# Kernel tuning notes

Hardware: AMD Instinct MI355X
Metric: run time of the kernel (lower is better)

The kernel has to match this reference:

```python
import jax, jax.numpy as jnp
import numpy as np

NODE_F = 8      # node_features
HID = 128       # hidden_dim
HEADS = 8       # nn.MultiheadAttention num_heads
OUT = 256       # output_dim
MAX_ATOMS = 4096  # max_pocket_atoms
NEIGHBOR_RADIUS = 3.0   # _compute_surface_scores neighbor_radius


def setup_inputs() -> dict:
    key = jax.random.key(0)
    ks = jax.random.split(key, 16)
    N, M = 16384, 32
    x = jax.random.normal(ks[0], (N, NODE_F), dtype=jnp.float32)
    pos = jax.random.normal(ks[1], (N, 3), dtype=jnp.float32) * 10.0
    ligand_pos = jax.random.normal(ks[2], (M, 3), dtype=jnp.float32) * 3.0

    def lin(k, fan_in, fan_out):
        return jax.random.normal(k, (fan_in, fan_out), dtype=jnp.float32) / np.sqrt(fan_in)

    return {
        'x': x, 'pos': pos, 'ligand_pos': ligand_pos,
        'W_node': lin(ks[3], NODE_F, HID), 'b_node': jnp.zeros((HID,), jnp.float32),
        'Wq': lin(ks[4], HID, HID), 'bq': jnp.zeros((HID,), jnp.float32),
        'Wk': lin(ks[5], HID, HID), 'bk': jnp.zeros((HID,), jnp.float32),
        'Wv': lin(ks[6], HID, HID), 'bv': jnp.zeros((HID,), jnp.float32),
        'Wo': lin(ks[7], HID, HID), 'bo': jnp.zeros((HID,), jnp.float32),
        'W1': lin(ks[8], HID, OUT), 'b1': jnp.zeros((OUT,), jnp.float32),
        'W2': lin(ks[9], OUT, OUT), 'b2': jnp.zeros((OUT,), jnp.float32),
    }


def _select_binding_site(pos, ligand_pos, k):
    # select_by_binding_site_proximity: distance-to-ligand-center + surface scores, topk
    lig_center = jnp.mean(ligand_pos, axis=0)                       # [3]
    d_lig = jnp.linalg.norm(pos - lig_center, axis=1)               # [N]
    # _compute_surface_scores: cdist(pos,pos) < 3.0, count neighbors (minus self)
    sq = jnp.sum(pos * pos, axis=1)                                 # [N]
    d2 = sq[:, None] + sq[None, :] - 2.0 * (pos @ pos.T)            # [N,N] squared distances
    neighbor_counts = jnp.sum(d2 < NEIGHBOR_RADIUS ** 2, axis=1) - 1
    surface = 1.0 / (neighbor_counts.astype(jnp.float32) + 1.0)
    scores = 1.0 / (1.0 + d_lig / 5.0) + 0.5 * surface
    _, idx = jax.lax.top_k(scores, k)                               # largest=True
    return idx


def reference(x, pos, ligand_pos, W_node, b_node, Wq, bq, Wk, bk, Wv, bv, Wo, bo, W1, b1, W2, b2):
    # N > max_pocket_atoms -> smart selection (adaptive with ligand_pos => binding_site)
    idx = _select_binding_site(pos, ligand_pos, MAX_ATOMS)
    xs = x[idx]                                                     # [K, NODE_F]

    # node embedding (E3 net call fails in the original -> h = node_embedding(x))
    h = xs @ W_node + b_node                                        # [K, HID]

    # MultiheadAttention over the single (batch=None) sequence, eval mode (no dropout)
    K = MAX_ATOMS
    dh = HID // HEADS
    q = (h @ Wq + bq).reshape(K, HEADS, dh).transpose(1, 0, 2)      # [H,K,dh]
    k_ = (h @ Wk + bk).reshape(K, HEADS, dh).transpose(1, 0, 2)
    v = (h @ Wv + bv).reshape(K, HEADS, dh).transpose(1, 0, 2)
    attn = jax.nn.softmax(jnp.einsum('hqd,hkd->hqk', q, k_) / np.sqrt(dh), axis=-1)
    av = jnp.einsum('hqk,hkd->hqd', attn, v).transpose(1, 0, 2).reshape(K, HID)
    h_att = av @ Wo + bo                                            # [K, HID]

    # global mean pool + output projection (Linear-ReLU-Linear)
    pooled = jnp.mean(h_att, axis=0)                                # [HID]
    out = jax.nn.relu(pooled @ W1 + b1) @ W2 + b2                   # [OUT]
    return out
```

## Files before the change

kernel.cpp:

```cpp
#include <hip/hip_runtime.h>
#include <cstdint>
#include <cstddef>

#define NPTS 16384
#define KSEL 4096
#define HIDDEN 128
#define NHEADS 8
#define DHEAD 16
#define OUTD 256
#define NSLICE 4
#define FCAP 262144
#define LCAP 2048
#define TAU 0.15f

typedef __attribute__((ext_vector_type(8))) short bf16x8;
typedef __attribute__((ext_vector_type(4))) float f32x4;
typedef __attribute__((ext_vector_type(16))) float f32x16;

#if defined(__has_builtin)
#if __has_builtin(__builtin_amdgcn_exp2f)
#define E2(x) __builtin_amdgcn_exp2f(x)
#endif
#endif
#ifndef E2
#define E2(x) exp2f(x)
#endif

constexpr size_t OFF_PA    = 1024;
constexpr size_t OFF_PB    = OFF_PA  + (size_t)NPTS*32;
constexpr size_t OFF_SQ    = OFF_PB  + (size_t)NPTS*32;
constexpr size_t OFF_DL    = OFF_SQ  + (size_t)NPTS*4;
constexpr size_t OFF_CNT   = OFF_DL  + (size_t)NPTS*4;
constexpr size_t OFF_NFLAG = OFF_CNT + (size_t)NPTS*4;
constexpr size_t OFF_FLG   = OFF_NFLAG + 1024;
constexpr size_t OFF_SEL   = OFF_FLG + (size_t)FCAP*4;
constexpr size_t SZ_PK     = (size_t)NHEADS*KSEL*32*2;
constexpr size_t OFF_QPK   = OFF_SEL + (size_t)KSEL*4;
constexpr size_t OFF_KPK   = OFF_QPK + SZ_PK;
constexpr size_t OFF_V     = OFF_KPK + SZ_PK;
constexpr size_t OFF_LP    = OFF_V  + (size_t)KSEL*HIDDEN*4;
constexpr size_t OFF_WP    = OFF_LP + (size_t)NHEADS*KSEL*NSLICE*4;
constexpr size_t OFF_PAV   = OFF_WP + (size_t)NHEADS*KSEL*NSLICE*4;

__device__ __forceinline__ unsigned short f2bf(float f) {
    union { float f; unsigned u; } v; v.f = f;
    unsigned r = v.u + 0x7fffu + ((v.u >> 16) & 1u);
    return (unsigned short)(r >> 16);
}
__device__ __forceinline__ float bf2f(unsigned short h) {
    union { unsigned u; float f; } v; v.u = ((unsigned)h) << 16;
    return v.f;
}

__global__ void __launch_bounds__(256) k_prep(const float* __restrict__ pos, const float* __restrict__ lig, int M,
                       unsigned short* __restrict__ pa, unsigned short* __restrict__ pb,
                       float* __restrict__ sq, float* __restrict__ dl,
                       int* __restrict__ cnt, unsigned int* __restrict__ nflag, float* __restrict__ pav) {
    __shared__ float ls[128];
    __shared__ float ctr[3];
    int tid = threadIdx.x;
    int i = blockIdx.x * 256 + tid;
    cnt[i] = 0;
    if (i == 0) *nflag = 0;
    if (blockIdx.x == 0 && tid < HIDDEN) pav[tid] = 0.f;
    for (int k = tid; k < 3 * M; k += 256) ls[k] = lig[k];
    __syncthreads();
    if (tid < 3) {
        float s = 0.f;
        for (int k = 0; k < M; k++) s += ls[k * 3 + tid];
        ctr[tid] = s / (float)M;
    }
    __syncthreads();
    float x = pos[i*3+0], y = pos[i*3+1], z = pos[i*3+2];
    float s = (x*x + y*y) + z*z;
    sq[i] = s;
    float dx = x - ctr[0], dy = y - ctr[1], dz = z - ctr[2];
    dl[i] = sqrtf((dx*dx + dy*dy) + dz*dz);
    unsigned short xh = f2bf(x); float xr = bf2f(xh); float xl = x - xr;
    unsigned short yh = f2bf(y); float yr = bf2f(yh); float yl = y - yr;
    unsigned short zh = f2bf(z); float zr = bf2f(zh); float zl = z - zr;
    unsigned short xlb = f2bf(xl), ylb = f2bf(yl), zlb = f2bf(zl);
    unsigned short xhA = f2bf(-2.f*xr), xlA = f2bf(-2.f*xl);
    unsigned short yhA = f2bf(-2.f*yr), ylA = f2bf(-2.f*yl);
    unsigned short zhA = f2bf(-2.f*zr), zlA = f2bf(-2.f*zl);
    unsigned short sih = f2bf(s);
    unsigned short sil = f2bf(s - bf2f(sih));
    unsigned short one = f2bf(1.0f);
    union { unsigned short s[16]; float4 f[2]; } A, B;
    A.s[0]=xhA; A.s[1]=xhA; A.s[2]=xlA;
    A.s[3]=yhA; A.s[4]=yhA; A.s[5]=ylA;
    A.s[6]=zhA; A.s[7]=zhA; A.s[8]=zlA;
    A.s[9]=xlA; A.s[10]=ylA; A.s[11]=zlA;
    A.s[12]=sih; A.s[13]=sil; A.s[14]=one; A.s[15]=one;
    B.s[0]=xh;  B.s[1]=xlb;  B.s[2]=xh;
    B.s[3]=yh;  B.s[4]=ylb;  B.s[5]=yh;
    B.s[6]=zh;  B.s[7]=zlb;  B.s[8]=zh;
    B.s[9]=xlb; B.s[10]=ylb; B.s[11]=zlb;
    B.s[12]=one; B.s[13]=one; B.s[14]=sih; B.s[15]=sil;
    float4* pad = (float4*)(pa + (size_t)i * 16);
    pad[0] = A.f[0]; pad[1] = A.f[1];
    float4* pbd = (float4*)(pb + (size_t)i * 16);
    pbd[0] = B.f[0]; pbd[1] = B.f[1];
}

__global__ void __launch_bounds__(256) k_neighbor(
        const unsigned short* __restrict__ pa, const unsigned short* __restrict__ pb,
        int* __restrict__ cnt, unsigned int* __restrict__ flg, unsigned int* __restrict__ nflag) {
    __shared__ unsigned short js[256 * 24];
    __shared__ unsigned int fbuf[LCAP];
    __shared__ unsigned int fcnt, fbase;
    int tid = threadIdx.x;
    if (tid == 0) fcnt = 0;
    int lane = tid & 63, w = tid >> 6;
    int half = lane >> 5, il = lane & 31;
    int i = blockIdx.x * 128 + w * 32 + il;
    bf16x8 bfrag = *(const bf16x8*)(pb + (size_t)i * 16 + half * 8);
    int jb0 = blockIdx.y * 1024;
    int acc = 0;
    for (int chv = 0; chv < 4; chv++) {
        int jb = jb0 + chv * 256;
        __syncthreads();
        {
            const float4* src = (const float4*)(pa + (size_t)(jb + tid) * 16);
            float4 v0 = src[0], v1 = src[1];
            float4* dst = (float4*)&js[tid * 24];
            dst[0] = v0; dst[1] = v1;
        }
        __syncthreads();
        #pragma unroll 2
        for (int t = 0; t < 8; t++) {
            bf16x8 afrag = *(const bf16x8*)&js[(t * 32 + il) * 24 + half * 8];
            f32x16 c = {0.f,0.f,0.f,0.f,0.f,0.f,0.f,0.f,0.f,0.f,0.f,0.f,0.f,0.f,0.f,0.f};
            c = __builtin_amdgcn_mfma_f32_32x32x16_bf16(afrag, bfrag, c, 0, 0, 0);
            int cs = 0, cl = 0;
            #pragma unroll
            for (int r = 0; r < 16; r++) {
                cs += (c[r] < 9.0f - TAU);
                cl += (c[r] < 9.0f + TAU);
            }
            if (cl == cs) {
                acc += cs;
            } else {
                unsigned jt9 = (unsigned)((jb >> 5) + t);
                unsigned xx = atomicAdd(&fcnt, 1u);
                if (xx < LCAP) fbuf[xx] = ((unsigned)i << 10) | (jt9 << 1) | (unsigned)half;
            }
        }
    }
    acc += __shfl_xor(acc, 32);
    if (half == 0) atomicAdd(&cnt[i], acc);
    __syncthreads();
    if (tid == 0) {
        unsigned cf = fcnt; if (cf > LCAP) cf = LCAP;
        fcnt = cf;
        fbase = atomicAdd(nflag, cf);
    }
    __syncthreads();
    unsigned cf = fcnt, fb = fbase;
    for (unsigned xx = tid; xx < cf; xx += 256) {
        unsigned di = fb + xx;
        if (di < FCAP) flg[di] = fbuf[xx];
    }
}

__global__ void __launch_bounds__(256) k_fixup(const float* __restrict__ pos, const float* __restrict__ sq,
        const unsigned int* __restrict__ flg, const unsigned int* __restrict__ nflag,
        int* __restrict__ cnt) {
    int nf = (int)*nflag; if (nf > FCAP) nf = FCAP;
    for (int idx = blockIdx.x * 256 + threadIdx.x; idx < nf; idx += gridDim.x * 256) {
        unsigned pr = flg[idx];
        int i = (int)(pr >> 10);
        int jt = (int)((pr >> 1) & 511u) << 5;
        int half = (int)(pr & 1u);
        float xi = pos[i*3+0], yi = pos[i*3+1], zi = pos[i*3+2];
        float si = sq[i];
        int add = 0;
        #pragma unroll
        for (int r = 0; r < 16; r++) {
            int j = jt + (r & 3) + 8 * (r >> 2) + 4 * half;
            float xj = pos[j*3+0], yj = pos[j*3+1], zj = pos[j*3+2];
            float dot = fmaf(xi, xj, fmaf(yi, yj, zi * zj));
            float d2 = (si + sq[j]) - 2.0f * dot;
            add += (d2 < 9.0f);
        }
        atomicAdd(&cnt[i], add);
    }
}

__global__ void __launch_bounds__(1024) k_select(const float* __restrict__ dl, const int* __restrict__ cnt,
                                                 int* __restrict__ sel) {
    __shared__ unsigned int sk[NPTS];
    __shared__ int hist[256];
    __shared__ int scan2[256];
    __shared__ unsigned int s_prefix;
    __shared__ int s_rem, s_eqtot, s_nout, s_digit, s_cgt;
    int tid = threadIdx.x;
    for (int i = tid; i < NPTS; i += 1024) {
        float score = 1.0f / (1.0f + dl[i] / 5.0f) + 0.5f * (1.0f / (float)cnt[i]);
        unsigned int u = __float_as_uint(score);
        sk[i] = u ^ ((u & 0x80000000u) ? 0xFFFFFFFFu : 0x80000000u);
    }
    if (tid == 0) { s_prefix = 0; s_rem = KSEL; s_nout = 0; s_eqtot = 0; }
    __syncthreads();
    for (int p = 0; p < 4; p++) {
        int sh = 24 - 8 * p;
        if (tid < 256) hist[tid] = 0;
        __syncthreads();
        unsigned int pref = s_prefix;
        int shp = (p == 0) ? 0 : (32 - 8 * p);
        for (int i = tid; i < NPTS; i += 1024) {
            unsigned int key = sk[i];
            bool m = (p == 0) || ((key >> shp) == pref);
            if (m) atomicAdd(&hist[(key >> sh) & 255], 1);
        }
        __syncthreads();
        if (tid < 256) scan2[tid] = hist[tid];
        __syncthreads();
        for (int off = 1; off < 256; off <<= 1) {
            int v = 0;
            if (tid < 256) { v = scan2[tid]; if (tid + off < 256) v += scan2[tid + off]; }
            __syncthreads();
            if (tid < 256) scan2[tid] = v;
            __syncthreads();
        }
        int rem = s_rem;
        if (tid < 256) {
            int hi = scan2[tid];
            int lo = hi - hist[tid];
            if (hi >= rem && lo < rem) { s_digit = tid; s_cgt = lo; }
        }
        __syncthreads();
        if (tid == 0) {
            s_prefix = (s_prefix << 8) | (unsigned int)s_digit;
            s_rem = rem - s_cgt;
            if (p == 3) s_eqtot = hist[s_digit];
        }
        __syncthreads();
    }
    unsigned int T = s_prefix;
    int need_eq = s_rem;
    for (int i = tid; i < NPTS; i += 1024)
        if (sk[i] > T) sel[atomicAdd(&s_nout, 1)] = i;
    __syncthreads();
    if (s_eqtot == need_eq) {
        for (int i = tid; i < NPTS; i += 1024)
            if (sk[i] == T) sel[atomicAdd(&s_nout, 1)] = i;
    } else {
        for (int i = tid; i < NPTS; i += 1024) {
            if (sk[i] == T) {
                int rank = 0;
                for (int j = 0; j < i; j++) rank += (sk[j] == T);
                if (rank < need_eq) sel[atomicAdd(&s_nout, 1)] = i;
            }
        }
    }
}

__global__ void __launch_bounds__(256) k_qkv(const float* __restrict__ x, const int* __restrict__ sel,
        const float* __restrict__ Wn, const float* __restrict__ bn,
        const float* __restrict__ Wq, const float* __restrict__ bq,
        const float* __restrict__ Wk, const float* __restrict__ bk,
        const float* __restrict__ Wv, const float* __restrict__ bv,
        unsigned short* __restrict__ qpk, unsigned short* __restrict__ kpk,
        float* __restrict__ vg) {
    __shared__ float xs[32][8];
    __shared__ __align__(16) float hs[32][HIDDEN];
    int tid = threadIdx.x;
    int r0 = blockIdx.x * 32;
    { int rr = tid >> 3, cc = tid & 7; xs[rr][cc] = x[(size_t)sel[r0 + rr] * 8 + cc]; }
    __syncthreads();
    int d = tid & 127, hr = tid >> 7;
    {
        float wn[8];
        #pragma unroll
        for (int c = 0; c < 8; c++) wn[c] = Wn[c * HIDDEN + d];
        float b = bn[d];
        #pragma unroll
        for (int r = 0; r < 16; r++) {
            int row = hr * 16 + r;
            float a = b;
            #pragma unroll
            for (int c = 0; c < 8; c++) a = fmaf(xs[row][c], wn[c], a);
            hs[row][d] = a;
        }
    }
    __syncthreads();
    int hh = d >> 4, dd = d & 15;
    float acc[16];
    {
        float b = bq[d];
        #pragma unroll
        for (int r = 0; r < 16; r++) acc[r] = b;
        for (int c = 0; c < HIDDEN; c += 4) {
            float w0 = Wq[(c+0)*HIDDEN+d], w1 = Wq[(c+1)*HIDDEN+d], w2 = Wq[(c+2)*HIDDEN+d], w3 = Wq[(c+3)*HIDDEN+d];
            #pragma unroll
            for (int r = 0; r < 16; r++) {
                float4 h4 = *(const float4*)&hs[hr*16+r][c];
                float a = acc[r];
                a = fmaf(h4.x, w0, a); a = fmaf(h4.y, w1, a); a = fmaf(h4.z, w2, a); a = fmaf(h4.w, w3, a);
                acc[r] = a;
            }
        }
        #pragma unroll
        for (int r = 0; r < 16; r++) {
            float val = acc[r] * 0.36067376022224085f;
            unsigned short hi = f2bf(val);
            unsigned short lo = f2bf(val - bf2f(hi));
            size_t idx = ((size_t)(hh * KSEL) + r0 + hr*16 + r) * 32 + dd;
            qpk[idx] = hi; qpk[idx + 16] = lo;
        }
    }
    {
        float b = bk[d];
        #pragma unroll
        for (int r = 0; r < 16; r++) acc[r] = b;
        for (int c = 0; c < HIDDEN; c += 4) {
            float w0 = Wk[(c+0)*HIDDEN+d], w1 = Wk[(c+1)*HIDDEN+d], w2 = Wk[(c+2)*HIDDEN+d], w3 = Wk[(c+3)*HIDDEN+d];
            #pragma unroll
            for (int r = 0; r < 16; r++) {
                float4 h4 = *(const float4*)&hs[hr*16+r][c];
                float a = acc[r];
                a = fmaf(h4.x, w0, a); a = fmaf(h4.y, w1, a); a = fmaf(h4.z, w2, a); a = fmaf(h4.w, w3, a);
                acc[r] = a;
            }
        }
        #pragma unroll
        for (int r = 0; r < 16; r++) {
            float val = acc[r];
            unsigned short hi = f2bf(val);
            unsigned short lo = f2bf(val - bf2f(hi));
            size_t idx = ((size_t)(hh * KSEL) + r0 + hr*16 + r) * 32 + dd;
            kpk[idx] = hi; kpk[idx + 16] = lo;
        }
    }
    {
        float b = bv[d];
        #pragma unroll
        for (int r = 0; r < 16; r++) acc[r] = b;
        for (int c = 0; c < HIDDEN; c += 4) {
            float w0 = Wv[(c+0)*HIDDEN+d], w1 = Wv[(c+1)*HIDDEN+d], w2 = Wv[(c+2)*HIDDEN+d], w3 = Wv[(c+3)*HIDDEN+d];
            #pragma unroll
            for (int r = 0; r < 16; r++) {
                float4 h4 = *(const float4*)&hs[hr*16+r][c];
                float a = acc[r];
                a = fmaf(h4.x, w0, a); a = fmaf(h4.y, w1, a); a = fmaf(h4.z, w2, a); a = fmaf(h4.w, w3, a);
                acc[r] = a;
            }
        }
        #pragma unroll
        for (int r = 0; r < 16; r++) vg[(size_t)(r0 + hr*16 + r) * HIDDEN + d] = acc[r];
    }
}

__global__ void __launch_bounds__(256) k_attn_l(
        const unsigned short* __restrict__ qpk, const unsigned short* __restrict__ kpk,
        float* __restrict__ lp) {
    __shared__ unsigned short smem[256 * 40];
    int tid = threadIdx.x;
    int ks = blockIdx.x, yg = blockIdx.y, h = blockIdx.z;
    size_t hb = (size_t)h * KSEL;
    int lane = tid & 63, w = tid >> 6;
    int n = lane & 15, g = lane >> 4;
    int q0w = yg * 64 + w * 16;
    bf16x8 afrag = *(const bf16x8*)(qpk + (hb + q0w + n) * 32 + g * 8);
    float l0 = 0.f, l1 = 0.f, l2 = 0.f, l3 = 0.f;
    int b1off = (g & 1) * 8;
    int b2off = 16 + g * 8;
    for (int kc = 0; kc < 4; kc++) {
        __syncthreads();
        {
            int krow = ks * 1024 + kc * 256 + tid;
            const float4* src = (const float4*)(kpk + (hb + krow) * 32);
            float4 a0 = src[0], a1 = src[1], a2 = src[2], a3 = src[3];
            float4* dst = (float4*)&smem[tid * 40];
            dst[0] = a0; dst[1] = a1; dst[2] = a2; dst[3] = a3;
        }
        __syncthreads();
        #pragma unroll 4
        for (int t = 0; t < 16; t++) {
            const unsigned short* rowp = &smem[(t * 16 + n) * 40];
            bf16x8 b1 = *(const bf16x8*)(rowp + b1off);
            bf16x8 b2 = {0,0,0,0,0,0,0,0};
            if (g < 2) b2 = *(const bf16x8*)(rowp + b2off);
            f32x4 c = {0.f, 0.f, 0.f, 0.f};
            c = __builtin_amdgcn_mfma_f32_16x16x32_bf16(afrag, b1, c, 0, 0, 0);
            c = __builtin_amdgcn_mfma_f32_16x16x32_bf16(afrag, b2, c, 0, 0, 0);
            l0 += E2(c[0]); l1 += E2(c[1]); l2 += E2(c[2]); l3 += E2(c[3]);
        }
    }
    #pragma unroll
    for (int m = 1; m < 16; m <<= 1) {
        l0 += __shfl_xor(l0, m); l1 += __shfl_xor(l1, m);
        l2 += __shfl_xor(l2, m); l3 += __shfl_xor(l3, m);
    }
    if (n == 0) {
        size_t base = (hb + q0w + g * 4) * NSLICE + ks;
        lp[base]            = l0; lp[base + NSLICE]     = l1;
        lp[base + 2*NSLICE] = l2; lp[base + 3*NSLICE]   = l3;
    }
}

__global__ void __launch_bounds__(256) k_attn_w(
        const unsigned short* __restrict__ qpk, const unsigned short* __restrict__ kpk,
        const float* __restrict__ lp, float* __restrict__ wp) {
    __shared__ unsigned short smem[256 * 40];
    __shared__ float rls[256];
    int tid = threadIdx.x;
    int qs = blockIdx.x, yg = blockIdx.y, h = blockIdx.z;
    size_t hb = (size_t)h * KSEL;
    int lane = tid & 63, w = tid >> 6;
    int n = lane & 15, g = lane >> 4;
    int j0w = yg * 64 + w * 16;
    bf16x8 afrag = *(const bf16x8*)(kpk + (hb + j0w + n) * 32 + g * 8);
    float w0 = 0.f, w1 = 0.f, w2 = 0.f, w3 = 0.f;
    int b1off = (g & 1) * 8;
    int b2off = 16 + g * 8;
    for (int qc = 0; qc < 4; qc++) {
        __syncthreads();
        {
            int qrow = qs * 1024 + qc * 256 + tid;
            const float4* src = (const float4*)(qpk + (hb + qrow) * 32);
            float4 a0 = src[0], a1 = src[1], a2 = src[2], a3 = src[3];
            float4* dst = (float4*)&smem[tid * 40];
            dst[0] = a0; dst[1] = a1; dst[2] = a2; dst[3] = a3;
            float4 p = ((const float4*)lp)[hb + qrow];
            rls[tid] = 1.0f / ((p.x + p.y) + (p.z + p.w));
        }
        __syncthreads();
        #pragma unroll 4
        for (int t = 0; t < 16; t++) {
            const unsigned short* rowp = &smem[(t * 16 + n) * 40];
            bf16x8 b1 = *(const bf16x8*)(rowp + b1off);
            bf16x8 b2 = {0,0,0,0,0,0,0,0};
            if (g < 2) b2 = *(const bf16x8*)(rowp + b2off);
            f32x4 c = {0.f, 0.f, 0.f, 0.f};
            c = __builtin_amdgcn_mfma_f32_16x16x32_bf16(afrag, b1, c, 0, 0, 0);
            c = __builtin_amdgcn_mfma_f32_16x16x32_bf16(afrag, b2, c, 0, 0, 0);
            float rv = rls[t * 16 + n];
            w0 = fmaf(E2(c[0]), rv, w0); w1 = fmaf(E2(c[1]), rv, w1);
            w2 = fmaf(E2(c[2]), rv, w2); w3 = fmaf(E2(c[3]), rv, w3);
        }
    }
    #pragma unroll
    for (int m = 1; m < 16; m <<= 1) {
        w0 += __shfl_xor(w0, m); w1 += __shfl_xor(w1, m);
        w2 += __shfl_xor(w2, m); w3 += __shfl_xor(w3, m);
    }
    if (n == 0) {
        size_t base = (hb + j0w + g * 4) * NSLICE + qs;
        wp[base]            = w0; wp[base + NSLICE]     = w1;
        wp[base + 2*NSLICE] = w2; wp[base + 3*NSLICE]   = w3;
    }
}

__global__ void __launch_bounds__(256) k_colsum(const float* __restrict__ wp, const float* __restrict__ vg,
                                                float* __restrict__ pav) {
    __shared__ float wl[NHEADS][32];
    __shared__ float red[128];
    int tid = threadIdx.x;
    int j0 = blockIdx.x * 32;
    {
        int h = tid >> 5, jl = tid & 31;
        float4 p = ((const float4*)wp)[(size_t)h * KSEL + j0 + jl];
        wl[h][jl] = (p.x + p.y) + (p.z + p.w);
    }
    __syncthreads();
    int d = tid & 127, g = tid >> 7;
    int h = d >> 4;
    float acc = 0.f;
    for (int jl = g * 16; jl < g * 16 + 16; jl++)
        acc = fmaf(wl[h][jl], vg[(size_t)(j0 + jl) * HIDDEN + d], acc);
    if (g == 1) red[d] = acc;
    __syncthreads();
    if (g == 0) atomicAdd(&pav[d], (acc + red[d]) * (1.0f / (float)KSEL));
}

__global__ void __launch_bounds__(256) k_final(const float* __restrict__ pav,
        const float* __restrict__ Wo, const float* __restrict__ bo,
        const float* __restrict__ W1, const float* __restrict__ b1,
        const float* __restrict__ W2, const float* __restrict__ b2,
        float* __restrict__ out) {
    __shared__ float sp[HIDDEN];
    __shared__ float st[OUTD];
    int t = threadIdx.x;
    if (t < HIDDEN) {
        float a = bo[t];
        for (int c = 0; c < HIDDEN; c++) a = fmaf(pav[c], Wo[c * HIDDEN + t], a);
        sp[t] = a;
    }
    __syncthreads();
    {
        float a = b1[t];
        for (int c = 0; c < HIDDEN; c++) a = fmaf(sp[c], W1[c * OUTD + t], a);
        st[t] = fmaxf(a, 0.f);
    }
    __syncthreads();
    {
        float o = b2[t];
        for (int c = 0; c < OUTD; c++) o = fmaf(st[c], W2[c * OUTD + t], o);
        out[t] = o;
    }
}

extern "C" void kernel_launch(void* const* d_in, const int* in_sizes, int n_in,
                              void* d_out, int out_size, void* d_ws, size_t ws_size,
                              hipStream_t stream) {
    (void)n_in; (void)out_size; (void)ws_size;
    const float* x   = (const float*)d_in[0];
    const float* pos = (const float*)d_in[1];
    const float* lig = (const float*)d_in[2];
    const float* Wn  = (const float*)d_in[3];
    const float* bn  = (const float*)d_in[4];
    const float* Wq  = (const float*)d_in[5];
    const float* bq  = (const float*)d_in[6];
    const float* Wk  = (const float*)d_in[7];
    const float* bk  = (const float*)d_in[8];
    const float* Wv  = (const float*)d_in[9];
    const float* bv  = (const float*)d_in[10];
    const float* Wo  = (const float*)d_in[11];
    const float* bo  = (const float*)d_in[12];
    const float* W1  = (const float*)d_in[13];
    const float* b1  = (const float*)d_in[14];
    const float* W2  = (const float*)d_in[15];
    const float* b2  = (const float*)d_in[16];
    int M = in_sizes[2] / 3;

    char* ws = (char*)d_ws;
    unsigned short* pa  = (unsigned short*)(ws + OFF_PA);
    unsigned short* pb  = (unsigned short*)(ws + OFF_PB);
    float*          sq  = (float*)(ws + OFF_SQ);
    float*          dl  = (float*)(ws + OFF_DL);
    int*            cnt = (int*)  (ws + OFF_CNT);
    unsigned int*   nfl = (unsigned int*)(ws + OFF_NFLAG);
    unsigned int*   flg = (unsigned int*)(ws + OFF_FLG);
    int*            sel = (int*)  (ws + OFF_SEL);
    unsigned short* qpk = (unsigned short*)(ws + OFF_QPK);
    unsigned short* kpk = (unsigned short*)(ws + OFF_KPK);
    float*          vg  = (float*)(ws + OFF_V);
    float*          lp  = (float*)(ws + OFF_LP);
    float*          wp  = (float*)(ws + OFF_WP);
    float*          pav = (float*)(ws + OFF_PAV);

    hipLaunchKernelGGL(k_prep,     dim3(64),       dim3(256),  0, stream, pos, lig, M, pa, pb, sq, dl, cnt, nfl, pav);
    hipLaunchKernelGGL(k_neighbor, dim3(128, 16),  dim3(256),  0, stream, pa, pb, cnt, flg, nfl);
    hipLaunchKernelGGL(k_fixup,    dim3(128),      dim3(256),  0, stream, pos, sq, flg, nfl, cnt);
    hipLaunchKernelGGL(k_select,   dim3(1),        dim3(1024), 0, stream, dl, cnt, sel);
    hipLaunchKernelGGL(k_qkv,      dim3(KSEL/32),  dim3(256),  0, stream, x, sel, Wn, bn, Wq, bq, Wk, bk, Wv, bv, qpk, kpk, vg);
    hipLaunchKernelGGL(k_attn_l,   dim3(4, 64, 8), dim3(256),  0, stream, qpk, kpk, lp);
    hipLaunchKernelGGL(k_attn_w,   dim3(4, 64, 8), dim3(256),  0, stream, qpk, kpk, lp, wp);
    hipLaunchKernelGGL(k_colsum,   dim3(KSEL/32),  dim3(256),  0, stream, wp, vg, pav);
    hipLaunchKernelGGL(k_final,    dim3(1),        dim3(256),  0, stream, pav, Wo, bo, W1, b1, W2, b2, (float*)d_out);
}
```

Before: 285.5 us.

## Compute QKV projections with bf16 split-precision MFMA instead of scalar FMA

Adds a kernel that pre-splits Wq/Wk/Wv into transposed hi/lo bf16 pairs. k_qkv now stores the embedded rows as hi/lo bf16 in shared memory and runs 16x16x32 bf16 MFMAs over the concatenated hi|lo dimension, which approximates fp32 with three cross terms. The grid also splits the three projections across blockIdx.y, giving three times as many blocks. This replaces the scalar fp32 FMA loops with matrix-core work, at the cost of an extra launch and a small loss of precision from dropping the lo*lo term.

```diff
diff --git a/kernel.cpp b/kernel.cpp
--- a/kernel.cpp
+++ b/kernel.cpp
@@ -12,6 +12,7 @@
 #define FCAP 262144
 #define LCAP 2048
 #define TAU 0.15f
+#define HROW 264
 
 typedef __attribute__((ext_vector_type(8))) short bf16x8;
 typedef __attribute__((ext_vector_type(4))) float f32x4;
@@ -41,6 +42,7 @@
 constexpr size_t OFF_LP    = OFF_V  + (size_t)KSEL*HIDDEN*4;
 constexpr size_t OFF_WP    = OFF_LP + (size_t)NHEADS*KSEL*NSLICE*4;
 constexpr size_t OFF_PAV   = OFF_WP + (size_t)NHEADS*KSEL*NSLICE*4;
+constexpr size_t OFF_WSP   = OFF_PAV + 1024;
 
 __device__ __forceinline__ unsigned short f2bf(float f) {
     union { float f; unsigned u; } v; v.f = f;
@@ -103,6 +105,20 @@
     pbd[0] = B.f[0]; pbd[1] = B.f[1];
 }
 
+__global__ void __launch_bounds__(256) k_wsplit(const float* __restrict__ Wq, const float* __restrict__ Wk,
+                                                const float* __restrict__ Wv, unsigned short* __restrict__ wsp) {
+    const float* W = (blockIdx.x == 0) ? Wq : ((blockIdx.x == 1) ? Wk : Wv);
+    unsigned short* dst = wsp + (size_t)blockIdx.x * HIDDEN * 256;
+    for (int idx = threadIdx.x; idx < HIDDEN * HIDDEN; idx += 256) {
+        int k = idx >> 7, n = idx & 127;
+        float w = W[k * HIDDEN + n];
+        unsigned short hi = f2bf(w);
+        unsigned short lo = f2bf(w - bf2f(hi));
+        dst[(size_t)n * 256 + k] = hi;
+        dst[(size_t)n * 256 + 128 + k] = lo;
+    }
+}
+
 __global__ void __launch_bounds__(256) k_neighbor(
         const unsigned short* __restrict__ pa, const unsigned short* __restrict__ pb,
         int* __restrict__ cnt, unsigned int* __restrict__ flg, unsigned int* __restrict__ nflag) {
@@ -258,97 +274,86 @@
 
 __global__ void __launch_bounds__(256) k_qkv(const float* __restrict__ x, const int* __restrict__ sel,
         const float* __restrict__ Wn, const float* __restrict__ bn,
-        const float* __restrict__ Wq, const float* __restrict__ bq,
-        const float* __restrict__ Wk, const float* __restrict__ bk,
-        const float* __restrict__ Wv, const float* __restrict__ bv,
+        const float* __restrict__ bq, const float* __restrict__ bk, const float* __restrict__ bv,
+        const unsigned short* __restrict__ wsp,
         unsigned short* __restrict__ qpk, unsigned short* __restrict__ kpk,
         float* __restrict__ vg) {
     __shared__ float xs[32][8];
-    __shared__ __align__(16) float hs[32][HIDDEN];
+    __shared__ unsigned short hsp[32 * HROW];
     int tid = threadIdx.x;
     int r0 = blockIdx.x * 32;
+    int proj = blockIdx.y;
     { int rr = tid >> 3, cc = tid & 7; xs[rr][cc] = x[(size_t)sel[r0 + rr] * 8 + cc]; }
     __syncthreads();
-    int d = tid & 127, hr = tid >> 7;
     {
+        int d = tid & 127, rp = tid >> 7;
         float wn[8];
         #pragma unroll
         for (int c = 0; c < 8; c++) wn[c] = Wn[c * HIDDEN + d];
         float b = bn[d];
-        #pragma unroll
-        for (int r = 0; r < 16; r++) {
-            int row = hr * 16 + r;
+        for (int r = rp; r < 32; r += 2) {
             float a = b;
             #pragma unroll
-            for (int c = 0; c < 8; c++) a = fmaf(xs[row][c], wn[c], a);
-            hs[row][d] = a;
-        }
-    }
-    __syncthreads();
-    int hh = d >> 4, dd = d & 15;
-    float acc[16];
-    {
-        float b = bq[d];
+            for (int c = 0; c < 8; c++) a = fmaf(xs[r][c], wn[c], a);
+            unsigned short hi = f2bf(a);
+            unsigned short lo = f2bf(a - bf2f(hi));
+            hsp[r * HROW + d] = hi;
+            hsp[r * HROW + 128 + d] = lo;
+        }
+    }
+    __syncthreads();
+    int lane = tid & 63, w = tid >> 6;
+    int n = lane & 15, g = lane >> 4;
+    int rloc = (w & 1) * 16;
+    int chalf = w >> 1;
+    const unsigned short* wb = wsp + (size_t)proj * HIDDEN * 256;
+    const unsigned short* arow = &hsp[(rloc + n) * HROW + ((g < 2) ? 0 : 128) + (g & 1) * 8];
+    int b1off = (g & 1) * 8;
+    for (int tc = 0; tc < 4; tc++) {
+        int col0 = chalf * 64 + tc * 16;
+        const unsigned short* bcol = wb + (size_t)(col0 + n) * 256;
+        f32x4 acc = {0.f, 0.f, 0.f, 0.f};
         #pragma unroll
-        for (int r = 0; r < 16; r++) acc[r] = b;
-        for (int c = 0; c < HIDDEN; c += 4) {
-            float w0 = Wq[(c+0)*HIDDEN+d], w1 = Wq[(c+1)*HIDDEN+d], w2 = Wq[(c+2)*HIDDEN+d], w3 = Wq[(c+3)*HIDDEN+d];
+        for (int c = 0; c < 8; c++) {
+            bf16x8 af = *(const bf16x8*)(arow + c * 16);
+            bf16x8 b1 = *(const bf16x8*)(bcol + c * 16 + b1off);
+            bf16x8 b2 = {0,0,0,0,0,0,0,0};
+            if (g < 2) b2 = *(const bf16x8*)(bcol + 128 + c * 16 + b1off);
+            acc = __builtin_amdgcn_mfma_f32_16x16x32_bf16(af, b1, acc, 0, 0, 0);
+            acc = __builtin_amdgcn_mfma_f32_16x16x32_bf16(af, b2, acc, 0, 0, 0);
+        }
+        int col = col0 + n;
+        int hh = col >> 4, dd = col & 15;
+        if (proj == 0) {
+            float bb = bq[col];
             #pragma unroll
-            for (int r = 0; r < 16; r++) {
-                float4 h4 = *(const float4*)&hs[hr*16+r][c];
-                float a = acc[r];
-                a = fmaf(h4.x, w0, a); a = fmaf(h4.y, w1, a); a = fmaf(h4.z, w2, a); a = fmaf(h4.w, w3, a);
-                acc[r] = a;
+            for (int r = 0; r < 4; r++) {
+                int qrow = r0 + rloc + g * 4 + r;
+                float val = (acc[r] + bb) * 0.36067376022224085f;
+                unsigned short hi = f2bf(val);
+                unsigned short lo = f2bf(val - bf2f(hi));
+                size_t idx = ((size_t)(hh * KSEL) + qrow) * 32 + dd;
+                qpk[idx] = hi; qpk[idx + 16] = lo;
             }
-        }
-        #pragma unroll
-        for (int r = 0; r < 16; r++) {
-            float val = acc[r] * 0.36067376022224085f;
-            unsigned short hi = f2bf(val);
-            unsigned short lo = f2bf(val - bf2f(hi));
-            size_t idx = ((size_t)(hh * KSEL) + r0 + hr*16 + r) * 32 + dd;
-            qpk[idx] = hi; qpk[idx + 16] = lo;
-        }
-    }
-    {
-        float b = bk[d];
-        #pragma unroll
-        for (int r = 0; r < 16; r++) acc[r] = b;
-        for (int c = 0; c < HIDDEN; c += 4) {
-            float w0 = Wk[(c+0)*HIDDEN+d], w1 = Wk[(c+1)*HIDDEN+d], w2 = Wk[(c+2)*HIDDEN+d], w3 = Wk[(c+3)*HIDDEN+d];
+        } else if (proj == 1) {
+            float bb = bk[col];
             #pragma unroll
-            for (int r = 0; r < 16; r++) {
-                float4 h4 = *(const float4*)&hs[hr*16+r][c];
-                float a = acc[r];
-                a = fmaf(h4.x, w0, a); a = fmaf(h4.y, w1, a); a = fmaf(h4.z, w2, a); a = fmaf(h4.w, w3, a);
-                acc[r] = a;
+            for (int r = 0; r < 4; r++) {
+                int qrow = r0 + rloc + g * 4 + r;
+                float val = acc[r] + bb;
+                unsigned short hi = f2bf(val);
+                unsigned short lo = f2bf(val - bf2f(hi));
+                size_t idx = ((size_t)(hh * KSEL) + qrow) * 32 + dd;
+                kpk[idx] = hi; kpk[idx + 16] = lo;
             }
-        }
-        #pragma unroll
-        for (int r = 0; r < 16; r++) {
-            float val = acc[r];
-            unsigned short hi = f2bf(val);
-            unsigned short lo = f2bf(val - bf2f(hi));
-            size_t idx = ((size_t)(hh * KSEL) + r0 + hr*16 + r) * 32 + dd;
-            kpk[idx] = hi; kpk[idx + 16] = lo;
-        }
-    }
-    {
-        float b = bv[d];
-        #pragma unroll
-        for (int r = 0; r < 16; r++) acc[r] = b;
-        for (int c = 0; c < HIDDEN; c += 4) {
-            float w0 = Wv[(c+0)*HIDDEN+d], w1 = Wv[(c+1)*HIDDEN+d], w2 = Wv[(c+2)*HIDDEN+d], w3 = Wv[(c+3)*HIDDEN+d];
+        } else {
+            float bb = bv[col];
             #pragma unroll
-            for (int r = 0; r < 16; r++) {
-                float4 h4 = *(const float4*)&hs[hr*16+r][c];
-                float a = acc[r];
-                a = fmaf(h4.x, w0, a); a = fmaf(h4.y, w1, a); a = fmaf(h4.z, w2, a); a = fmaf(h4.w, w3, a);
-                acc[r] = a;
+            for (int r = 0; r < 4; r++) {
+                int qrow = r0 + rloc + g * 4 + r;
+                vg[(size_t)qrow * HIDDEN + col] = acc[r] + bb;
             }
         }
-        #pragma unroll
-        for (int r = 0; r < 16; r++) vg[(size_t)(r0 + hr*16 + r) * HIDDEN + d] = acc[r];
     }
 }
 
@@ -540,12 +545,14 @@
     float*          lp  = (float*)(ws + OFF_LP);
     float*          wp  = (float*)(ws + OFF_WP);
     float*          pav = (float*)(ws + OFF_PAV);
+    unsigned short* wsp = (unsigned short*)(ws + OFF_WSP);
 
     hipLaunchKernelGGL(k_prep,     dim3(64),       dim3(256),  0, stream, pos, lig, M, pa, pb, sq, dl, cnt, nfl, pav);
+    hipLaunchKernelGGL(k_wsplit,   dim3(3),        dim3(256),  0, stream, Wq, Wk, Wv, wsp);
     hipLaunchKernelGGL(k_neighbor, dim3(128, 16),  dim3(256),  0, stream, pa, pb, cnt, flg, nfl);
     hipLaunchKernelGGL(k_fixup,    dim3(128),      dim3(256),  0, stream, pos, sq, flg, nfl, cnt);
     hipLaunchKernelGGL(k_select,   dim3(1),        dim3(1024), 0, stream, dl, cnt, sel);
-    hipLaunchKernelGGL(k_qkv,      dim3(KSEL/32),  dim3(256),  0, stream, x, sel, Wn, bn, Wq, bq, Wk, bk, Wv, bv, qpk, kpk, vg);
+    hipLaunchKernelGGL(k_qkv,      dim3(128, 3),   dim3(256),  0, stream, x, sel, Wn, bn, bq, bk, bv, wsp, qpk, kpk, vg);
     hipLaunchKernelGGL(k_attn_l,   dim3(4, 64, 8), dim3(256),  0, stream, qpk, kpk, lp);
     hipLaunchKernelGGL(k_attn_w,   dim3(4, 64, 8), dim3(256),  0, stream, qpk, kpk, lp, wp);
     hipLaunchKernelGGL(k_colsum,   dim3(KSEL/32),  dim3(256),  0, stream, wp, vg, pav);
```

New measurement: 288.1 us. About the same (+0.9%).
